# Performance work log

Hardware: AMD Instinct MI355X
Metric: run time of the kernel (lower is better)

The kernel has to match this reference:

```python
import jax, jax.numpy as jnp
import numpy as np

N = 100_000      # nodes
E = 3_200_000    # edges (avg degree 32)
G = 512          # graphs in batch
IN_DIM = 3
H = 64
L = 3
BN_EPS = 1e-5


def setup_inputs() -> dict:
    key = jax.random.key(0)
    ks = jax.random.split(key, 14)
    s = 0.1
    x = jax.random.normal(ks[0], (N, IN_DIM), jnp.float32)
    edge_index = jax.random.randint(ks[1], (2, E), 0, N, dtype=jnp.int32)
    batch = jnp.sort(jax.random.randint(ks[2], (N,), 0, G, dtype=jnp.int32))
    # GIN MLP params per layer: Linear(in,H) -> ReLU -> Linear(H,H)
    w1_0 = jax.random.normal(ks[3], (IN_DIM, H), jnp.float32) * s   # layer 0 first linear
    w1_r = jax.random.normal(ks[4], (L - 1, H, H), jnp.float32) * s  # layers 1..L-1 first linear
    b1 = jax.random.normal(ks[5], (L, H), jnp.float32) * s
    w2 = jax.random.normal(ks[6], (L, H, H), jnp.float32) * s
    b2 = jax.random.normal(ks[7], (L, H), jnp.float32) * s
    gamma = 1.0 + jax.random.normal(ks[8], (L, H), jnp.float32) * 0.05
    beta = jax.random.normal(ks[9], (L, H), jnp.float32) * 0.05
    wout = jax.random.normal(ks[10], (H, H), jnp.float32) * s
    bout = jax.random.normal(ks[11], (H,), jnp.float32) * s
    return {"x": x, "edge_index": edge_index, "batch": batch,
            "w1_0": w1_0, "w1_r": w1_r, "b1": b1, "w2": w2, "b2": b2,
            "gamma": gamma, "beta": beta, "wout": wout, "bout": bout}


def reference(x, edge_index, batch, w1_0, w1_r, b1, w2, b2, gamma, beta, wout, bout):
    src, dst = edge_index[0], edge_index[1]
    for i in range(L):
        # GINConv: h = mlp((1+eps)*x + sum_{j in N(i)} x_j), eps = 0
        agg = jax.ops.segment_sum(x[src], dst, num_segments=N)  # [N, d]
        h = x + agg
        W1 = w1_0 if i == 0 else w1_r[i - 1]
        h = jax.nn.relu(h @ W1 + b1[i]) @ w2[i] + b2[i]          # [N, H]
        # BatchNorm1d (training mode: biased batch stats over nodes)
        mu = h.mean(axis=0)
        var = h.var(axis=0)
        h = (h - mu) / jnp.sqrt(var + BN_EPS) * gamma[i] + beta[i]
        x = jax.nn.relu(h)
    # global_mean_pool: segment mean over graph ids
    sums = jax.ops.segment_sum(x, batch, num_segments=G)                        # [G, H]
    cnt = jax.ops.segment_sum(jnp.ones((N, 1), x.dtype), batch, num_segments=G)  # [G, 1]
    graph_repr = jnp.where(cnt > 0, sums / jnp.maximum(cnt, 1.0), 0.0)
    return graph_repr @ wout + bout  # [G, H]
```

## Files before the change

kernel.cpp:

```cpp
#include <hip/hip_runtime.h>


#define NBMAX 1024
#define CAP 4608
#define CHUNK 8192

typedef __attribute__((ext_vector_type(8))) short bf16x8;
typedef __attribute__((ext_vector_type(4))) float f32x4;

static __device__ __forceinline__ bf16x8 as_bf16x8(uint4 u) {
    union { uint4 a; bf16x8 b; } x; x.a = u; return x.b;
}
static __device__ __forceinline__ unsigned short bf16r(float v) {
    unsigned u = __float_as_uint(v);
    return (unsigned short)((u + 0x7FFFu + ((u >> 16) & 1u)) >> 16);
}
static __device__ __forceinline__ unsigned bf16pack2(float a, float b) {
    return (unsigned)bf16r(a) | ((unsigned)bf16r(b) << 16);
}

__global__ void prep_weights(const float* __restrict__ w1_0, const float* __restrict__ w1_r,
                             const float* __restrict__ w2, unsigned short* __restrict__ w1T0,
                             unsigned short* __restrict__ w1T, unsigned short* __restrict__ w2T) {
    int t = blockIdx.x * 256 + threadIdx.x;
    if (t < 64 * 32) {
        int c = t >> 5, k = t & 31;
        w1T0[t] = bf16r(k < 3 ? w1_0[k * 64 + c] : 0.f);
    }
    if (t < 2 * 64 * 64) {
        int l = t >> 12, r = t & 4095, c = r >> 6, k = r & 63;
        w1T[t] = bf16r(w1_r[l * 4096 + k * 64 + c]);
    }
    if (t < 3 * 64 * 64) {
        int l = t >> 12, r = t & 4095, c = r >> 6, k = r & 63;
        w2T[t] = bf16r(w2[l * 4096 + k * 64 + c]);
    }
}

__global__ __launch_bounds__(512) void bucket_scatter(
    const int* __restrict__ src, const int* __restrict__ dst,
    int* __restrict__ cursor, int* __restrict__ bucketed, int E) {
    __shared__ int h[NBMAX];
    __shared__ int base[NBMAX];
    int t = threadIdx.x;
    for (int i = t; i < NBMAX; i += 512) h[i] = 0;
    __syncthreads();
    int e0 = blockIdx.x * CHUNK, e1 = min(e0 + CHUNK, E);
    for (int e = e0 + t; e < e1; e += 512) atomicAdd(&h[dst[e] >> 7], 1);
    __syncthreads();
    for (int i = t; i < NBMAX; i += 512) {
        int v = h[i];
        base[i] = v ? atomicAdd(&cursor[i], v) : 0;
        h[i] = 0;
    }
    __syncthreads();
    for (int e = e0 + t; e < e1; e += 512) {
        int d = dst[e];
        int bk = d >> 7;
        int r = base[bk] + atomicAdd(&h[bk], 1);
        if (r < CAP) bucketed[bk * CAP + r] = src[e] | ((d & 127) << 20);
    }
}

__global__ __launch_bounds__(256) void bucket_csr(
    int* __restrict__ bucketed, const int* __restrict__ bcnt,
    int* __restrict__ rowstart, int* __restrict__ rowend, int N) {
    __shared__ int ein[CAP];
    __shared__ int eout[CAP];
    __shared__ int hist[128];
    __shared__ int base[129];
    int b = blockIdx.x, t = threadIdx.x;
    int s = b * CAP, node0 = b << 7;
    int cnt = min(bcnt[b], CAP);
    if (t < 128) hist[t] = 0;
    __syncthreads();
    for (int j = t; j < cnt; j += 256) {
        int p = bucketed[s + j];
        ein[j] = p;
        atomicAdd(&hist[p >> 20], 1);
    }
    __syncthreads();
    if (t < 128) base[t + 1] = hist[t];
    if (t == 0) base[0] = 0;
    __syncthreads();
    for (int off = 1; off < 128; off <<= 1) {
        int v = 0;
        if (t < 128 && (t + 1) > off) v = base[t + 1 - off];
        __syncthreads();
        if (t < 128 && (t + 1) > off) base[t + 1] += v;
        __syncthreads();
    }
    if (t < 128) {
        int n = node0 + t;
        if (n < N) {
            rowstart[n] = s + base[t];
            rowend[n] = s + base[t + 1];
        }
        hist[t] = 0;
    }
    __syncthreads();
    for (int j = t; j < cnt; j += 256) {
        int p = ein[j];
        int local = p >> 20;
        int pos = base[local] + atomicAdd(&hist[local], 1);
        eout[pos] = p & 0xFFFFF;
    }
    __syncthreads();
    for (int j = t; j < cnt; j += 256) bucketed[s + j] = eout[j];
}

__global__ void agg3(const float* __restrict__ x, const int* __restrict__ rowstart,
                     const int* __restrict__ rowend, const int* __restrict__ csr,
                     uint4* __restrict__ out, int N) {
    int n = blockIdx.x * blockDim.x + threadIdx.x;
    if (n >= N) return;
    float a0 = x[n * 3], a1 = x[n * 3 + 1], a2 = x[n * 3 + 2];
    float b0 = 0.f, b1 = 0.f, b2 = 0.f;
    float c0 = 0.f, c1 = 0.f, c2 = 0.f;
    float d0 = 0.f, d1 = 0.f, d2 = 0.f;
    int s = rowstart[n], e = rowend[n];
    int j = s;
    for (; j + 3 < e; j += 4) {
        int i0 = csr[j], i1 = csr[j + 1], i2 = csr[j + 2], i3 = csr[j + 3];
        a0 += x[i0 * 3]; a1 += x[i0 * 3 + 1]; a2 += x[i0 * 3 + 2];
        b0 += x[i1 * 3]; b1 += x[i1 * 3 + 1]; b2 += x[i1 * 3 + 2];
        c0 += x[i2 * 3]; c1 += x[i2 * 3 + 1]; c2 += x[i2 * 3 + 2];
        d0 += x[i3 * 3]; d1 += x[i3 * 3 + 1]; d2 += x[i3 * 3 + 2];
    }
    for (; j < e; j++) {
        int nb = csr[j];
        a0 += x[nb * 3]; a1 += x[nb * 3 + 1]; a2 += x[nb * 3 + 2];
    }
    float s0 = a0 + b0 + c0 + d0, s1 = a1 + b1 + c1 + d1, s2 = a2 + b2 + c2 + d2;
    out[n] = make_uint4(bf16pack2(s0, s1), bf16pack2(s2, 0.f), 0u, 0u);
}

__device__ __forceinline__ void accum_bf16(const uint4 u,
                                           const float4 scA, const float4 scB,
                                           const float4 shA, const float4 shB,
                                           float* __restrict__ a) {
    a[0] += fmaxf(__uint_as_float(u.x << 16) * scA.x + shA.x, 0.f);
    a[1] += fmaxf(__uint_as_float(u.x & 0xFFFF0000u) * scA.y + shA.y, 0.f);
    a[2] += fmaxf(__uint_as_float(u.y << 16) * scA.z + shA.z, 0.f);
    a[3] += fmaxf(__uint_as_float(u.y & 0xFFFF0000u) * scA.w + shA.w, 0.f);
    a[4] += fmaxf(__uint_as_float(u.z << 16) * scB.x + shB.x, 0.f);
    a[5] += fmaxf(__uint_as_float(u.z & 0xFFFF0000u) * scB.y + shB.y, 0.f);
    a[6] += fmaxf(__uint_as_float(u.w << 16) * scB.z + shB.z, 0.f);
    a[7] += fmaxf(__uint_as_float(u.w & 0xFFFF0000u) * scB.w + shB.w, 0.f);
}

__global__ __launch_bounds__(256) void agg64_bn(
    const unsigned short* __restrict__ h, const int* __restrict__ rowstart,
    const int* __restrict__ rowend, const int* __restrict__ csr,
    const float* __restrict__ bnsum, const float* __restrict__ bnsq,
    const float* __restrict__ gamma, const float* __restrict__ beta,
    uint4* __restrict__ out, int N) {
    __shared__ float scs[64], shs[64];
    int t = threadIdx.x;
    if (t < 64) {
        float mu = bnsum[t] / (float)N;
        float var = bnsq[t] / (float)N - mu * mu;
        float s = gamma[t] * rsqrtf(var + 1e-5f);
        scs[t] = s;
        shs[t] = beta[t] - mu * s;
    }
    __syncthreads();
    int g = t >> 3, l = t & 7;
    int n = blockIdx.x * 32 + g;
    if (n >= N) return;
    int c0 = l * 8;
    float4 scA = *(const float4*)&scs[c0], scB = *(const float4*)&scs[c0 + 4];
    float4 shA = *(const float4*)&shs[c0], shB = *(const float4*)&shs[c0 + 4];
    const uint4* hr = (const uint4*)h;
    float A[8] = {0,0,0,0,0,0,0,0};
    float B[8] = {0,0,0,0,0,0,0,0};
    uint4 self = hr[(size_t)n * 8 + l];
    accum_bf16(self, scA, scB, shA, shB, A);
    int s = rowstart[n], e = rowend[n];
    int j = s;
    for (; j + 3 < e; j += 4) {
        int i0 = csr[j], i1 = csr[j + 1], i2 = csr[j + 2], i3 = csr[j + 3];
        uint4 w0 = hr[(size_t)i0 * 8 + l];
        uint4 w1 = hr[(size_t)i1 * 8 + l];
        uint4 w2 = hr[(size_t)i2 * 8 + l];
        uint4 w3 = hr[(size_t)i3 * 8 + l];
        accum_bf16(w0, scA, scB, shA, shB, A);
        accum_bf16(w1, scA, scB, shA, shB, B);
        accum_bf16(w2, scA, scB, shA, shB, A);
        accum_bf16(w3, scA, scB, shA, shB, B);
    }
    for (; j < e; j++) {
        uint4 w = hr[(size_t)csr[j] * 8 + l];
        accum_bf16(w, scA, scB, shA, shB, A);
    }
    uint4 o;
    o.x = bf16pack2(A[0] + B[0], A[1] + B[1]);
    o.y = bf16pack2(A[2] + B[2], A[3] + B[3]);
    o.z = bf16pack2(A[4] + B[4], A[5] + B[5]);
    o.w = bf16pack2(A[6] + B[6], A[7] + B[7]);
    out[(size_t)n * 8 + l] = o;
}

template <bool L0>
__global__ __launch_bounds__(256) void mlp_mfma(
    const uint4* __restrict__ actIn,
    unsigned short* __restrict__ hout,
    const uint4* __restrict__ w1Tu,
    const float* __restrict__ b1,
    const uint4* __restrict__ w2Tu,
    const float* __restrict__ b2,
    float* __restrict__ bnsum, float* __restrict__ bnsq, int N) {
    __shared__ unsigned short mids[64 * 64];
    __shared__ float red[16][64];
    int t = threadIdx.x;
    int w = t >> 6, l = t & 63;
    int m16 = l & 15, q = l >> 4;
    float s[4] = {0, 0, 0, 0}, sq[4] = {0, 0, 0, 0};
    const uint4 z4 = make_uint4(0, 0, 0, 0);
    for (int base = blockIdx.x * 64; base < N; base += gridDim.x * 64) {
        __syncthreads();
        int rA = base + w * 16 + m16;
        bf16x8 a0, a1;
        if (L0) {
            a0 = as_bf16x8((rA < N && q == 0) ? actIn[rA] : z4);
        } else {
            a0 = as_bf16x8(rA < N ? actIn[(size_t)rA * 8 + q] : z4);
            a1 = as_bf16x8(rA < N ? actIn[(size_t)rA * 8 + 4 + q] : z4);
        }
        for (int c = 0; c < 4; c++) {
            int col = c * 16 + m16;
            float bias = b1[col];
            f32x4 acc = {bias, bias, bias, bias};
            if (L0) {
                bf16x8 bb0 = as_bf16x8(w1Tu[col * 4 + q]);
                acc = __builtin_amdgcn_mfma_f32_16x16x32_bf16(a0, bb0, acc, 0, 0, 0);
            } else {
                bf16x8 bb0 = as_bf16x8(w1Tu[col * 8 + q]);
                bf16x8 bb1 = as_bf16x8(w1Tu[col * 8 + 4 + q]);
                acc = __builtin_amdgcn_mfma_f32_16x16x32_bf16(a0, bb0, acc, 0, 0, 0);
                acc = __builtin_amdgcn_mfma_f32_16x16x32_bf16(a1, bb1, acc, 0, 0, 0);
            }
            int kb = col >> 3, ko = col & 7;
#pragma unroll
            for (int r = 0; r < 4; r++) {
                int row = w * 16 + q * 4 + r;
                mids[row * 64 + ((kb ^ (row & 7)) << 3) + ko] = bf16r(fmaxf(acc[r], 0.f));
            }
        }
        __syncthreads();
        int rowM = w * 16 + m16;
        const uint4* midU4 = (const uint4*)mids;
        bf16x8 a20 = as_bf16x8(midU4[rowM * 8 + (q ^ (rowM & 7))]);
        bf16x8 a21 = as_bf16x8(midU4[rowM * 8 + ((4 + q) ^ (rowM & 7))]);
        for (int c = 0; c < 4; c++) {
            int col = c * 16 + m16;
            float bias = b2[col];
            f32x4 acc = {bias, bias, bias, bias};
            bf16x8 bb0 = as_bf16x8(w2Tu[col * 8 + q]);
            bf16x8 bb1 = as_bf16x8(w2Tu[col * 8 + 4 + q]);
            acc = __builtin_amdgcn_mfma_f32_16x16x32_bf16(a20, bb0, acc, 0, 0, 0);
            acc = __builtin_amdgcn_mfma_f32_16x16x32_bf16(a21, bb1, acc, 0, 0, 0);
#pragma unroll
            for (int r = 0; r < 4; r++) {
                int row = base + w * 16 + q * 4 + r;
                if (row < N) {
                    float v = acc[r];
                    hout[(size_t)row * 64 + col] = bf16r(v);
                    s[c] += v;
                    sq[c] += v * v;
                }
            }
        }
    }
    __syncthreads();
    for (int c = 0; c < 4; c++) red[w * 4 + q][c * 16 + m16] = s[c];
    __syncthreads();
    if (t < 64) {
        float S = 0.f;
        for (int i = 0; i < 16; i++) S += red[i][t];
        atomicAdd(&bnsum[t], S);
    }
    __syncthreads();
    for (int c = 0; c < 4; c++) red[w * 4 + q][c * 16 + m16] = sq[c];
    __syncthreads();
    if (t < 64) {
        float S = 0.f;
        for (int i = 0; i < 16; i++) S += red[i][t];
        atomicAdd(&bnsq[t], S);
    }
}

__device__ __forceinline__ int lowb(const int* __restrict__ a, int n, int v) {
    int lo = 0, hi = n;
    while (lo < hi) {
        int m = (lo + hi) >> 1;
        if (a[m] < v) lo = m + 1; else hi = m;
    }
    return lo;
}

__global__ __launch_bounds__(256) void bn_pool_out(
    const unsigned short* __restrict__ h, const int* __restrict__ batch,
    const float* __restrict__ bnsum, const float* __restrict__ bnsq,
    const float* __restrict__ gamma, const float* __restrict__ beta,
    const float* __restrict__ wout, const float* __restrict__ bout,
    float* __restrict__ out, int N) {
    __shared__ float sc[64], sh[64];
    __shared__ float part[4][64];
    __shared__ float gr[64];
    __shared__ int range[2];
    int g = blockIdx.x, t = threadIdx.x;
    if (t < 64) {
        float mu = bnsum[t] / (float)N;
        float var = bnsq[t] / (float)N - mu * mu;
        float s = gamma[t] * rsqrtf(var + 1e-5f);
        sc[t] = s;
        sh[t] = beta[t] - mu * s;
    }
    if (t == 64) range[0] = lowb(batch, N, g);
    if (t == 65) range[1] = lowb(batch, N, g + 1);
    __syncthreads();
    int s0 = range[0], s1 = range[1];
    int col = t & 63, ro = t >> 6;
    float acc = 0.f;
    for (int n = s0 + ro; n < s1; n += 4) {
        float v = __uint_as_float(((unsigned)h[(size_t)n * 64 + col]) << 16);
        acc += fmaxf(v * sc[col] + sh[col], 0.f);
    }
    part[ro][col] = acc;
    __syncthreads();
    if (t < 64) {
        float S = part[0][t] + part[1][t] + part[2][t] + part[3][t];
        float c = (float)(s1 - s0);
        gr[t] = (c > 0.f) ? S / c : 0.f;
    }
    __syncthreads();
    if (t < 64) {
        float a = bout[t];
        for (int f = 0; f < 64; f++) a += gr[f] * wout[f * 64 + t];
        out[g * 64 + t] = a;
    }
}

extern "C" void kernel_launch(void* const* d_in, const int* in_sizes, int n_in,
                              void* d_out, int out_size, void* d_ws, size_t ws_size,
                              hipStream_t stream) {
    const float* x     = (const float*)d_in[0];
    const int*   ei    = (const int*)d_in[1];
    const int*   batch = (const int*)d_in[2];
    const float* w1_0  = (const float*)d_in[3];
    const float* w1_r  = (const float*)d_in[4];
    const float* b1    = (const float*)d_in[5];
    const float* w2    = (const float*)d_in[6];
    const float* b2    = (const float*)d_in[7];
    const float* gamma = (const float*)d_in[8];
    const float* beta  = (const float*)d_in[9];
    const float* wout  = (const float*)d_in[10];
    const float* bout  = (const float*)d_in[11];
    float* out = (float*)d_out;

    const int N = in_sizes[2];
    const int E = in_sizes[1] / 2;
    const int NB = (N + 127) >> 7;

    unsigned short* hbX = (unsigned short*)d_ws;
    unsigned short* hbY = hbX + (size_t)N * 64;
    uint4* h3b = (uint4*)(hbY + (size_t)N * 64);
    int* bucketed = (int*)(h3b + N);
    int* rowstart = bucketed + (size_t)NB * CAP;
    int* rowend   = rowstart + N;
    int* cursor   = rowend + N;
    float* bnstats = (float*)(cursor + NBMAX);
    unsigned short* w1T0 = (unsigned short*)(bnstats + 384);
    unsigned short* w1T  = w1T0 + 64 * 32;
    unsigned short* w2T  = w1T + 2 * 64 * 64;

    const int* srcv = ei;
    const int* dstv = ei + E;

    hipMemsetAsync(cursor, 0, (NBMAX + 384) * 4, stream);
    prep_weights<<<48, 256, 0, stream>>>(w1_0, w1_r, w2, w1T0, w1T, w2T);

    bucket_scatter<<<(E + CHUNK - 1) / CHUNK, 512, 0, stream>>>(srcv, dstv, cursor, bucketed, E);
    bucket_csr<<<NB, 256, 0, stream>>>(bucketed, cursor, rowstart, rowend, N);

    agg3<<<(N + 255) / 256, 256, 0, stream>>>(x, rowstart, rowend, bucketed, h3b, N);
    mlp_mfma<true><<<782, 256, 0, stream>>>(h3b, hbX, (const uint4*)w1T0, b1,
                                            (const uint4*)w2T, b2,
                                            bnstats, bnstats + 64, N);

    agg64_bn<<<(N + 31) / 32, 256, 0, stream>>>(hbX, rowstart, rowend, bucketed,
                                                bnstats, bnstats + 64, gamma, beta,
                                                (uint4*)hbY, N);
    mlp_mfma<false><<<782, 256, 0, stream>>>((const uint4*)hbY, hbX, (const uint4*)w1T,
                                             b1 + 64, (const uint4*)(w2T + 4096), b2 + 64,
                                             bnstats + 128, bnstats + 192, N);

    agg64_bn<<<(N + 31) / 32, 256, 0, stream>>>(hbX, rowstart, rowend, bucketed,
                                                bnstats + 128, bnstats + 192,
                                                gamma + 64, beta + 64, (uint4*)hbY, N);
    mlp_mfma<false><<<782, 256, 0, stream>>>((const uint4*)hbY, hbX,
                                             (const uint4*)(w1T + 4096), b1 + 128,
                                             (const uint4*)(w2T + 8192), b2 + 128,
                                             bnstats + 256, bnstats + 320, N);

    bn_pool_out<<<512, 256, 0, stream>>>(hbX, batch, bnstats + 256, bnstats + 320,
                                         gamma + 128, beta + 128, wout, bout, out, N);
}
```

Before: 405.4 us.

## Sort edges per chunk in shared memory and split BN from aggregation

The edge bucketing kernel now sorts each chunk locally in shared memory and writes it out contiguously, recording per-chunk bucket offsets. This replaces global cursor atomics and scattered global writes. bucket_csr then gathers each bucket's runs from every chunk. Separately, the fused BN+ReLU inside the 64-dim aggregation is moved into a standalone elementwise pass, so each neighbour gather no longer repeats the BN math, at the cost of an extra full read/write of the activations. The deterministic layout may also improve locality, but gathering runs serially per chunk in bucket_csr could be slow.

```diff
diff --git a/kernel.cpp b/kernel.cpp
--- a/kernel.cpp
+++ b/kernel.cpp
@@ -4,6 +4,7 @@
 #define NBMAX 1024
 #define CAP 4608
 #define CHUNK 8192
+#define NBLK_MAX 512
 
 typedef __attribute__((ext_vector_type(8))) short bf16x8;
 typedef __attribute__((ext_vector_type(4))) float f32x4;
@@ -37,48 +38,86 @@
     }
 }
 
-__global__ __launch_bounds__(512) void bucket_scatter(
+__global__ __launch_bounds__(512) void scatter_sort(
     const int* __restrict__ src, const int* __restrict__ dst,
-    int* __restrict__ cursor, int* __restrict__ bucketed, int E) {
-    __shared__ int h[NBMAX];
-    __shared__ int base[NBMAX];
-    int t = threadIdx.x;
-    for (int i = t; i < NBMAX; i += 512) h[i] = 0;
-    __syncthreads();
-    int e0 = blockIdx.x * CHUNK, e1 = min(e0 + CHUNK, E);
-    for (int e = e0 + t; e < e1; e += 512) atomicAdd(&h[dst[e] >> 7], 1);
-    __syncthreads();
-    for (int i = t; i < NBMAX; i += 512) {
-        int v = h[i];
-        base[i] = v ? atomicAdd(&cursor[i], v) : 0;
-        h[i] = 0;
-    }
-    __syncthreads();
+    int* __restrict__ bucketed2, int* __restrict__ offsTab, int E) {
+    __shared__ int hist[NBMAX];
+    __shared__ int offs[NBMAX];
+    __shared__ int stage[CHUNK];
+    int t = threadIdx.x, blk = blockIdx.x;
+    int e0 = blk * CHUNK, e1 = min(e0 + CHUNK, E);
+    int len = e1 - e0;
+    hist[t] = 0; hist[t + 512] = 0;
+    __syncthreads();
+    for (int e = e0 + t; e < e1; e += 512) atomicAdd(&hist[dst[e] >> 7], 1);
+    __syncthreads();
+    offs[t] = hist[t]; offs[t + 512] = hist[t + 512];
+    __syncthreads();
+    for (int off = 1; off < 1024; off <<= 1) {
+        int v0 = (t >= off) ? offs[t - off] : 0;
+        int v1 = offs[t + 512 - off];
+        __syncthreads();
+        offs[t] += v0;
+        offs[t + 512] += v1;
+        __syncthreads();
+    }
+    offs[t] -= hist[t]; offs[t + 512] -= hist[t + 512];
+    hist[t] = 0; hist[t + 512] = 0;
+    __syncthreads();
+    offsTab[blk * 1025 + t] = offs[t];
+    offsTab[blk * 1025 + t + 512] = offs[t + 512];
+    if (t == 0) offsTab[blk * 1025 + 1024] = len;
     for (int e = e0 + t; e < e1; e += 512) {
         int d = dst[e];
         int bk = d >> 7;
-        int r = base[bk] + atomicAdd(&h[bk], 1);
-        if (r < CAP) bucketed[bk * CAP + r] = src[e] | ((d & 127) << 20);
-    }
+        int r = offs[bk] + atomicAdd(&hist[bk], 1);
+        stage[r] = src[e] | ((d & 127) << 20);
+    }
+    __syncthreads();
+    for (int j = t; j < len; j += 512) bucketed2[e0 + j] = stage[j];
 }
 
 __global__ __launch_bounds__(256) void bucket_csr(
-    int* __restrict__ bucketed, const int* __restrict__ bcnt,
-    int* __restrict__ rowstart, int* __restrict__ rowend, int N) {
+    const int* __restrict__ bucketed2, const int* __restrict__ offsTab,
+    int* __restrict__ csrOut, int* __restrict__ rowstart, int* __restrict__ rowend,
+    int N, int nblk) {
     __shared__ int ein[CAP];
     __shared__ int eout[CAP];
+    __shared__ int runs[NBLK_MAX];
+    __shared__ int rbeg[NBLK_MAX];
     __shared__ int hist[128];
     __shared__ int base[129];
-    int b = blockIdx.x, t = threadIdx.x;
-    int s = b * CAP, node0 = b << 7;
-    int cnt = min(bcnt[b], CAP);
+    int b = blockIdx.x, t = threadIdx.x, node0 = b << 7;
+    for (int r = t; r < NBLK_MAX; r += 256) {
+        int l = 0, g0 = 0;
+        if (r < nblk) {
+            int beg = offsTab[r * 1025 + b];
+            int end = offsTab[r * 1025 + b + 1];
+            l = end - beg;
+            g0 = r * CHUNK + beg;
+        }
+        runs[r] = l;
+        rbeg[r] = g0;
+    }
+    __syncthreads();
+    for (int off = 1; off < NBLK_MAX; off <<= 1) {
+        int v0 = (t >= off) ? runs[t - off] : 0;
+        int v1 = (t + 256 >= off) ? runs[t + 256 - off] : 0;
+        __syncthreads();
+        runs[t] += v0;
+        runs[t + 256] += v1;
+        __syncthreads();
+    }
+    int cnt = min(runs[NBLK_MAX - 1], CAP);
+    for (int r = t; r < nblk; r += 256) {
+        int s0 = (r == 0) ? 0 : runs[r - 1];
+        int s1 = runs[r];
+        int g = rbeg[r];
+        for (int p = s0; p < s1 && p < CAP; p++) ein[p] = bucketed2[g + (p - s0)];
+    }
     if (t < 128) hist[t] = 0;
     __syncthreads();
-    for (int j = t; j < cnt; j += 256) {
-        int p = bucketed[s + j];
-        ein[j] = p;
-        atomicAdd(&hist[p >> 20], 1);
-    }
+    for (int j = t; j < cnt; j += 256) atomicAdd(&hist[ein[j] >> 20], 1);
     __syncthreads();
     if (t < 128) base[t + 1] = hist[t];
     if (t == 0) base[0] = 0;
@@ -93,8 +132,8 @@
     if (t < 128) {
         int n = node0 + t;
         if (n < N) {
-            rowstart[n] = s + base[t];
-            rowend[n] = s + base[t + 1];
+            rowstart[n] = b * CAP + base[t];
+            rowend[n] = b * CAP + base[t + 1];
         }
         hist[t] = 0;
     }
@@ -106,7 +145,7 @@
         eout[pos] = p & 0xFFFFF;
     }
     __syncthreads();
-    for (int j = t; j < cnt; j += 256) bucketed[s + j] = eout[j];
+    for (int j = t; j < cnt; j += 256) csrOut[b * CAP + j] = eout[j];
 }
 
 __global__ void agg3(const float* __restrict__ x, const int* __restrict__ rowstart,
@@ -135,64 +174,72 @@
     out[n] = make_uint4(bf16pack2(s0, s1), bf16pack2(s2, 0.f), 0u, 0u);
 }
 
-__device__ __forceinline__ void accum_bf16(const uint4 u,
-                                           const float4 scA, const float4 scB,
-                                           const float4 shA, const float4 shB,
-                                           float* __restrict__ a) {
-    a[0] += fmaxf(__uint_as_float(u.x << 16) * scA.x + shA.x, 0.f);
-    a[1] += fmaxf(__uint_as_float(u.x & 0xFFFF0000u) * scA.y + shA.y, 0.f);
-    a[2] += fmaxf(__uint_as_float(u.y << 16) * scA.z + shA.z, 0.f);
-    a[3] += fmaxf(__uint_as_float(u.y & 0xFFFF0000u) * scA.w + shA.w, 0.f);
-    a[4] += fmaxf(__uint_as_float(u.z << 16) * scB.x + shB.x, 0.f);
-    a[5] += fmaxf(__uint_as_float(u.z & 0xFFFF0000u) * scB.y + shB.y, 0.f);
-    a[6] += fmaxf(__uint_as_float(u.w << 16) * scB.z + shB.z, 0.f);
-    a[7] += fmaxf(__uint_as_float(u.w & 0xFFFF0000u) * scB.w + shB.w, 0.f);
-}
-
-__global__ __launch_bounds__(256) void agg64_bn(
-    const unsigned short* __restrict__ h, const int* __restrict__ rowstart,
-    const int* __restrict__ rowend, const int* __restrict__ csr,
+__global__ __launch_bounds__(256) void bn_relu(
+    const uint4* __restrict__ h, uint4* __restrict__ y,
     const float* __restrict__ bnsum, const float* __restrict__ bnsq,
-    const float* __restrict__ gamma, const float* __restrict__ beta,
-    uint4* __restrict__ out, int N) {
-    __shared__ float scs[64], shs[64];
+    const float* __restrict__ gamma, const float* __restrict__ beta, int N) {
+    __shared__ float sc[64], sh[64];
     int t = threadIdx.x;
     if (t < 64) {
         float mu = bnsum[t] / (float)N;
         float var = bnsq[t] / (float)N - mu * mu;
         float s = gamma[t] * rsqrtf(var + 1e-5f);
-        scs[t] = s;
-        shs[t] = beta[t] - mu * s;
-    }
-    __syncthreads();
+        sc[t] = s;
+        sh[t] = beta[t] - mu * s;
+    }
+    __syncthreads();
+    int idx = blockIdx.x * 256 + t;
+    if (idx >= N * 8) return;
+    int c0 = (idx & 7) * 8;
+    uint4 u = h[idx];
+    float4 scA = *(const float4*)&sc[c0], scB = *(const float4*)&sc[c0 + 4];
+    float4 shA = *(const float4*)&sh[c0], shB = *(const float4*)&sh[c0 + 4];
+    float v0 = fmaxf(__uint_as_float(u.x << 16) * scA.x + shA.x, 0.f);
+    float v1 = fmaxf(__uint_as_float(u.x & 0xFFFF0000u) * scA.y + shA.y, 0.f);
+    float v2 = fmaxf(__uint_as_float(u.y << 16) * scA.z + shA.z, 0.f);
+    float v3 = fmaxf(__uint_as_float(u.y & 0xFFFF0000u) * scA.w + shA.w, 0.f);
+    float v4 = fmaxf(__uint_as_float(u.z << 16) * scB.x + shB.x, 0.f);
+    float v5 = fmaxf(__uint_as_float(u.z & 0xFFFF0000u) * scB.y + shB.y, 0.f);
+    float v6 = fmaxf(__uint_as_float(u.w << 16) * scB.z + shB.z, 0.f);
+    float v7 = fmaxf(__uint_as_float(u.w & 0xFFFF0000u) * scB.w + shB.w, 0.f);
+    y[idx] = make_uint4(bf16pack2(v0, v1), bf16pack2(v2, v3),
+                        bf16pack2(v4, v5), bf16pack2(v6, v7));
+}
+
+__device__ __forceinline__ void addu4(const uint4 u, float* __restrict__ a) {
+    a[0] += __uint_as_float(u.x << 16);
+    a[1] += __uint_as_float(u.x & 0xFFFF0000u);
+    a[2] += __uint_as_float(u.y << 16);
+    a[3] += __uint_as_float(u.y & 0xFFFF0000u);
+    a[4] += __uint_as_float(u.z << 16);
+    a[5] += __uint_as_float(u.z & 0xFFFF0000u);
+    a[6] += __uint_as_float(u.w << 16);
+    a[7] += __uint_as_float(u.w & 0xFFFF0000u);
+}
+
+__global__ __launch_bounds__(256) void agg64(
+    const unsigned short* __restrict__ y, const int* __restrict__ rowstart,
+    const int* __restrict__ rowend, const int* __restrict__ csr,
+    uint4* __restrict__ out, int N) {
+    int t = threadIdx.x;
     int g = t >> 3, l = t & 7;
     int n = blockIdx.x * 32 + g;
     if (n >= N) return;
-    int c0 = l * 8;
-    float4 scA = *(const float4*)&scs[c0], scB = *(const float4*)&scs[c0 + 4];
-    float4 shA = *(const float4*)&shs[c0], shB = *(const float4*)&shs[c0 + 4];
-    const uint4* hr = (const uint4*)h;
+    const uint4* yr = (const uint4*)y;
     float A[8] = {0,0,0,0,0,0,0,0};
     float B[8] = {0,0,0,0,0,0,0,0};
-    uint4 self = hr[(size_t)n * 8 + l];
-    accum_bf16(self, scA, scB, shA, shB, A);
+    addu4(yr[(size_t)n * 8 + l], A);
     int s = rowstart[n], e = rowend[n];
     int j = s;
     for (; j + 3 < e; j += 4) {
         int i0 = csr[j], i1 = csr[j + 1], i2 = csr[j + 2], i3 = csr[j + 3];
-        uint4 w0 = hr[(size_t)i0 * 8 + l];
-        uint4 w1 = hr[(size_t)i1 * 8 + l];
-        uint4 w2 = hr[(size_t)i2 * 8 + l];
-        uint4 w3 = hr[(size_t)i3 * 8 + l];
-        accum_bf16(w0, scA, scB, shA, shB, A);
-        accum_bf16(w1, scA, scB, shA, shB, B);
-        accum_bf16(w2, scA, scB, shA, shB, A);
-        accum_bf16(w3, scA, scB, shA, shB, B);
-    }
-    for (; j < e; j++) {
-        uint4 w = hr[(size_t)csr[j] * 8 + l];
-        accum_bf16(w, scA, scB, shA, shB, A);
-    }
+        uint4 w0 = yr[(size_t)i0 * 8 + l];
+        uint4 w1 = yr[(size_t)i1 * 8 + l];
+        uint4 w2 = yr[(size_t)i2 * 8 + l];
+        uint4 w3 = yr[(size_t)i3 * 8 + l];
+        addu4(w0, A); addu4(w1, B); addu4(w2, A); addu4(w3, B);
+    }
+    for (; j < e; j++) addu4(yr[(size_t)csr[j] * 8 + l], A);
     uint4 o;
     o.x = bf16pack2(A[0] + B[0], A[1] + B[1]);
     o.y = bf16pack2(A[2] + B[2], A[3] + B[3]);
@@ -362,15 +409,17 @@
     const int N = in_sizes[2];
     const int E = in_sizes[1] / 2;
     const int NB = (N + 127) >> 7;
+    const int nblk = (E + CHUNK - 1) / CHUNK;
 
     unsigned short* hbX = (unsigned short*)d_ws;
     unsigned short* hbY = hbX + (size_t)N * 64;
     uint4* h3b = (uint4*)(hbY + (size_t)N * 64);
-    int* bucketed = (int*)(h3b + N);
-    int* rowstart = bucketed + (size_t)NB * CAP;
-    int* rowend   = rowstart + N;
-    int* cursor   = rowend + N;
-    float* bnstats = (float*)(cursor + NBMAX);
+    int* bucketed2 = (int*)(h3b + N);
+    int* offsTab   = bucketed2 + (size_t)nblk * CHUNK;
+    int* csrOut    = offsTab + (size_t)nblk * 1025;
+    int* rowstart  = csrOut + (size_t)NB * CAP;
+    int* rowend    = rowstart + N;
+    float* bnstats = (float*)(rowend + N);
     unsigned short* w1T0 = (unsigned short*)(bnstats + 384);
     unsigned short* w1T  = w1T0 + 64 * 32;
     unsigned short* w2T  = w1T + 2 * 64 * 64;
@@ -378,27 +427,28 @@
     const int* srcv = ei;
     const int* dstv = ei + E;
 
-    hipMemsetAsync(cursor, 0, (NBMAX + 384) * 4, stream);
+    hipMemsetAsync(bnstats, 0, 384 * 4, stream);
     prep_weights<<<48, 256, 0, stream>>>(w1_0, w1_r, w2, w1T0, w1T, w2T);
 
-    bucket_scatter<<<(E + CHUNK - 1) / CHUNK, 512, 0, stream>>>(srcv, dstv, cursor, bucketed, E);
-    bucket_csr<<<NB, 256, 0, stream>>>(bucketed, cursor, rowstart, rowend, N);
-
-    agg3<<<(N + 255) / 256, 256, 0, stream>>>(x, rowstart, rowend, bucketed, h3b, N);
+    scatter_sort<<<nblk, 512, 0, stream>>>(srcv, dstv, bucketed2, offsTab, E);
+    bucket_csr<<<NB, 256, 0, stream>>>(bucketed2, offsTab, csrOut, rowstart, rowend, N, nblk);
+
+    agg3<<<(N + 255) / 256, 256, 0, stream>>>(x, rowstart, rowend, csrOut, h3b, N);
     mlp_mfma<true><<<782, 256, 0, stream>>>(h3b, hbX, (const uint4*)w1T0, b1,
                                             (const uint4*)w2T, b2,
                                             bnstats, bnstats + 64, N);
 
-    agg64_bn<<<(N + 31) / 32, 256, 0, stream>>>(hbX, rowstart, rowend, bucketed,
-                                                bnstats, bnstats + 64, gamma, beta,
-                                                (uint4*)hbY, N);
-    mlp_mfma<false><<<782, 256, 0, stream>>>((const uint4*)hbY, hbX, (const uint4*)w1T,
+    bn_relu<<<(N * 8 + 255) / 256, 256, 0, stream>>>((const uint4*)hbX, (uint4*)hbY,
+                                                     bnstats, bnstats + 64, gamma, beta, N);
+    agg64<<<(N + 31) / 32, 256, 0, stream>>>(hbY, rowstart, rowend, csrOut, (uint4*)hbX, N);
+    mlp_mfma<false><<<782, 256, 0, stream>>>((const uint4*)hbX, hbY, (const uint4*)w1T,
                                              b1 + 64, (const uint4*)(w2T + 4096), b2 + 64,
                                              bnstats + 128, bnstats + 192, N);
 
-    agg64_bn<<<(N + 31) / 32, 256, 0, stream>>>(hbX, rowstart, rowend, bucketed,
-                                                bnstats + 128, bnstats + 192,
-                                                gamma + 64, beta + 64, (uint4*)hbY, N);
+    bn_relu<<<(N * 8 + 255) / 256, 256, 0, stream>>>((const uint4*)hbY, (uint4*)hbX,
+                                                     bnstats + 128, bnstats + 192,
+                                                     gamma + 64, beta + 64, N);
+    agg64<<<(N + 31) / 32, 256, 0, stream>>>(hbX, rowstart, rowend, csrOut, (uint4*)hbY, N);
     mlp_mfma<false><<<782, 256, 0, stream>>>((const uint4*)hbY, hbX,
                                              (const uint4*)(w1T + 4096), b1 + 128,
                                              (const uint4*)(w2T + 8192), b2 + 128,
```

Result: slower. 435.4 us (+7.4%).
